# Performance work log

Hardware: AMD Instinct MI355X
Metric: run time of the kernel (lower is better)

Reference implementation:

```python
import jax, jax.numpy as jnp
import numpy as np

# Production-scale perfect decision-tree ensemble (Hummingbird perf_tree_trav layout)
B, F, T, D, C = 16384, 256, 512, 7, 4  # batch, features, trees, internal levels below root, classes


def setup_inputs() -> dict:
    key = jax.random.key(0)
    k = jax.random.split(key, 6)
    total = T * (2 ** (D + 1) - 2)  # concatenated per-level node/bias tables, level l has T*2^l entries
    return {
        "x": jax.random.normal(k[0], (B, F), dtype=jnp.float32),
        "root_nodes": jax.random.randint(k[1], (T,), 0, F, dtype=jnp.int32),
        "root_biases": jax.random.normal(k[2], (T,), dtype=jnp.float32),
        "tree_indices": jnp.arange(T, dtype=jnp.int32) * 2,
        "nodes_flat": jax.random.randint(k[3], (total,), 0, F, dtype=jnp.int32),
        "biases_flat": jax.random.normal(k[4], (total,), dtype=jnp.float32),
        "leaf_nodes": jax.random.normal(k[5], (T * 2 ** (D + 1), C), dtype=jnp.float32),
    }


def reference(x, root_nodes, root_biases, tree_indices, nodes_flat, biases_flat, leaf_nodes):
    # Root level: compare each tree's root feature against its bias. decision_cond = less (lt).
    # tree_indices = t*2 offsets indices into the flat level-1 table of size 2T;
    # the offset doubles along with the level size via `2*idx + cond`.
    idx = (x[:, root_nodes] < root_biases).astype(jnp.int32) + tree_indices  # [B, T]
    off = 0
    for l in range(1, D + 1):  # static loop over tree depth
        size = T << l
        lvl_nodes = nodes_flat[off:off + size]
        lvl_biases = biases_flat[off:off + size]
        feat_idx = lvl_nodes[idx]                          # [B, T] feature ids for current nodes
        feats = jnp.take_along_axis(x, feat_idx, axis=1)   # [B, T] per-sample feature gather
        idx = 2 * idx + (feats < lvl_biases[idx]).astype(jnp.int32)
        off += size
    leaves = leaf_nodes[idx]                               # [B, T, C]
    return leaves.sum(axis=1)                              # [B, C]
```

## Files before the change

### kernel.cpp

```cpp
#include <hip/hip_runtime.h>
#include <hip/hip_fp16.h>

#define BB 16384
#define FF 256
#define TT 512
#define DD 7

constexpr int NR1 = TT * 2;
constexpr int NR3 = TT * 8;
constexpr int NR5 = TT * 32;
constexpr int NN7 = TT * 128;
constexpr int NTOT = NR1 + NR3 + NR5 + NN7 + NN7;

constexpr size_t OFF_R3   = (size_t)NR1 * 16;
constexpr size_t OFF_R5   = OFF_R3 + (size_t)NR3 * 16;
constexpr size_t OFF_N7   = OFF_R5 + (size_t)NR5 * 16;
constexpr size_t OFF_LP   = OFF_N7 + (size_t)NN7 * 8;
constexpr size_t OFF_PART = OFF_LP + (size_t)NN7 * 16;
constexpr size_t WS_NEED  = OFF_PART + (size_t)2 * BB * 4 * sizeof(float);

__global__ void pack_kernel(const int* __restrict__ nf, const float* __restrict__ bf,
                            const float4* __restrict__ leaf4,
                            int4* __restrict__ R1, int4* __restrict__ R3,
                            int4* __restrict__ R5, int2* __restrict__ N7,
                            uint4* __restrict__ LP) {
    const int i = blockIdx.x * 256 + threadIdx.x;
    if (i < NR1) {
        const int e0 = i, eC = 2 * TT + 2 * i;
        const int fp = (nf[e0] & 255) | ((nf[eC] & 255) << 8) | ((nf[eC + 1] & 255) << 16);
        R1[i] = make_int4(fp, __float_as_int(bf[e0]),
                          __float_as_int(bf[eC]), __float_as_int(bf[eC + 1]));
    } else if (i < NR1 + NR3) {
        const int r = i - NR1;
        const int e0 = 6 * TT + r, eC = 14 * TT + 2 * r;
        const int fp = (nf[e0] & 255) | ((nf[eC] & 255) << 8) | ((nf[eC + 1] & 255) << 16);
        R3[r] = make_int4(fp, __float_as_int(bf[e0]),
                          __float_as_int(bf[eC]), __float_as_int(bf[eC + 1]));
    } else if (i < NR1 + NR3 + NR5) {
        const int r = i - NR1 - NR3;
        const int e0 = 30 * TT + r, eC = 62 * TT + 2 * r;
        const int fp = (nf[e0] & 255) | ((nf[eC] & 255) << 8) | ((nf[eC + 1] & 255) << 16);
        R5[r] = make_int4(fp, __float_as_int(bf[e0]),
                          __float_as_int(bf[eC]), __float_as_int(bf[eC + 1]));
    } else if (i < NR1 + NR3 + NR5 + NN7) {
        const int r = i - NR1 - NR3 - NR5;
        const int e = 126 * TT + r;
        N7[r] = make_int2(nf[e] & 255, __float_as_int(bf[e]));
    } else if (i < NTOT) {
        const int j = i - NR1 - NR3 - NR5 - NN7;
        const float4 l0 = leaf4[2 * j], l1 = leaf4[2 * j + 1];
        const __half2 a = __floats2half2_rn(l0.x, l0.y), b = __floats2half2_rn(l0.z, l0.w);
        const __half2 c = __floats2half2_rn(l1.x, l1.y), d = __floats2half2_rn(l1.z, l1.w);
        uint4 w;
        w.x = *reinterpret_cast<const unsigned int*>(&a);
        w.y = *reinterpret_cast<const unsigned int*>(&b);
        w.z = *reinterpret_cast<const unsigned int*>(&c);
        w.w = *reinterpret_cast<const unsigned int*>(&d);
        LP[j] = w;
    }
}

__device__ __forceinline__ int step2(const int4 w, const int i,
                                     const float* __restrict__ x_s,
                                     const int xb, const int sz) {
    const float v0 = x_s[xb | ((w.x & 255) ^ sz)];
    const int   c0 = (v0 < __int_as_float(w.y)) ? 1 : 0;
    const int   fc = c0 ? ((w.x >> 16) & 255) : ((w.x >> 8) & 255);
    const float bc = c0 ? __int_as_float(w.w) : __int_as_float(w.z);
    const float vc = x_s[xb | (fc ^ sz)];
    const int   c1 = (vc < bc) ? 1 : 0;
    return 4 * i + 2 * c0 + c1;
}

__global__ __launch_bounds__(1024, 4)
void tree_traverse_big(const float* __restrict__ x,
                       const int*   __restrict__ root_nodes,
                       const float* __restrict__ root_biases,
                       const int4*  __restrict__ R1, const int4* __restrict__ R3g,
                       const int4*  __restrict__ R5, const int2* __restrict__ N7,
                       const uint4* __restrict__ LP,
                       float*       __restrict__ out)
{
    extern __shared__ float smem[];
    float* x_s = smem;
    int4*  r3s = (int4*)(smem + 16384);

    const int tid = threadIdx.x;
    const int s   = tid & 63;
    const int tg  = tid >> 6;
    const int s0  = blockIdx.x * 64;

    {
        const float4* xg = (const float4*)(x + (size_t)s0 * FF);
        const int r  = tid >> 4;
        const int v  = tid & 15;
        const int rz = r & 31;
        float* row = x_s + (r << 8);
        #pragma unroll
        for (int c = 0; c < 4; ++c) {
            const float4 q = xg[r * (FF / 4) + v + 16 * c];
            const int f0 = (v + 16 * c) * 4;
            row[(f0 + 0) ^ rz] = q.x;
            row[(f0 + 1) ^ rz] = q.y;
            row[(f0 + 2) ^ rz] = q.z;
            row[(f0 + 3) ^ rz] = q.w;
        }
        #pragma unroll
        for (int i = 0; i < NR3 / 1024; ++i)
            r3s[tid + i * 1024] = R3g[tid + i * 1024];
    }
    __syncthreads();

    const int xb = s << 8;
    const int sz = s & 31;
    float a0 = 0.f, a1 = 0.f, a2 = 0.f, a3 = 0.f;

    constexpr int TPT = TT / 16;
    constexpr int NP  = 8;
    constexpr int NJ  = TPT / NP;

    #pragma unroll 1
    for (int j = 0; j < NJ; ++j) {
        const int tbase = tg * TPT + j * NP;
        int p[NP];

        #pragma unroll
        for (int k = 0; k < NP; ++k) {
            const int tu = __builtin_amdgcn_readfirstlane(tbase + k);
            const int   rn  = root_nodes[tu];
            const float rbv = root_biases[tu];
            const int4  rA  = R1[2 * tu];
            const int4  rB  = R1[2 * tu + 1];
            const int c0 = (x_s[xb | (rn ^ sz)] < rbv) ? 1 : 0;
            int4 r;
            r.x = c0 ? rB.x : rA.x;  r.y = c0 ? rB.y : rA.y;
            r.z = c0 ? rB.z : rA.z;  r.w = c0 ? rB.w : rA.w;
            p[k] = step2(r, c0, x_s, xb, sz);
        }
        #pragma unroll
        for (int k = 0; k < NP; ++k)
            p[k] = step2(r3s[((tbase + k) << 3) + p[k]], p[k], x_s, xb, sz);
        #pragma unroll
        for (int k = 0; k < NP; ++k)
            p[k] = step2(R5[((tbase + k) << 5) + p[k]], p[k], x_s, xb, sz);
        #pragma unroll
        for (int k = 0; k < NP; ++k) {
            const int idx7 = ((tbase + k) << 7) + p[k];
            const int2  n  = N7[idx7];
            const uint4 lp = LP[idx7];
            const int c7 = (x_s[xb | (n.x ^ sz)] < __int_as_float(n.y)) ? 1 : 0;
            const unsigned int w01 = c7 ? lp.z : lp.x;
            const unsigned int w23 = c7 ? lp.w : lp.y;
            const float2 f01 = __half22float2(*reinterpret_cast<const __half2*>(&w01));
            const float2 f23 = __half22float2(*reinterpret_cast<const __half2*>(&w23));
            a0 += f01.x; a1 += f01.y; a2 += f23.x; a3 += f23.y;
        }
    }

    __syncthreads();
    ((float4*)x_s)[tid] = make_float4(a0, a1, a2, a3);
    __syncthreads();
    if (tid < 256) {
        float o = 0.f;
        #pragma unroll
        for (int g = 0; g < 16; ++g)
            o += x_s[(g << 8) + tid];
        out[(size_t)s0 * 4 + tid] = o;
    }
}

__global__ __launch_bounds__(1024, 8)
void tree_traverse_kernel(const float* __restrict__ x,
                          const int*   __restrict__ root_nodes,
                          const float* __restrict__ root_biases,
                          const int4*  __restrict__ R1, const int4* __restrict__ R3,
                          const int4*  __restrict__ R5, const int2* __restrict__ N7,
                          const uint4* __restrict__ LP,
                          float*       __restrict__ part)
{
    extern __shared__ float x_s[];
    const int tid = threadIdx.x;
    const int s   = tid & 63;
    const int tg  = tid >> 6;
    const int s0  = blockIdx.x * 64;
    const int h0  = blockIdx.y * (TT / 2);
    {
        const float4* xg = (const float4*)(x + (size_t)s0 * FF);
        const int r = tid >> 4, v = tid & 15, rz = r & 31;
        float* row = x_s + (r << 8);
        #pragma unroll
        for (int c = 0; c < 4; ++c) {
            const float4 q = xg[r * (FF / 4) + v + 16 * c];
            const int f0 = (v + 16 * c) * 4;
            row[(f0 + 0) ^ rz] = q.x; row[(f0 + 1) ^ rz] = q.y;
            row[(f0 + 2) ^ rz] = q.z; row[(f0 + 3) ^ rz] = q.w;
        }
    }
    __syncthreads();
    const int xb = s << 8, sz = s & 31;
    float a0 = 0.f, a1 = 0.f, a2 = 0.f, a3 = 0.f;
    constexpr int TPT = (TT / 2) / 16, NP = 8, NJ = TPT / NP;
    #pragma unroll 1
    for (int j = 0; j < NJ; ++j) {
        const int tbase = h0 + tg * TPT + j * NP;
        int p[NP];
        #pragma unroll
        for (int k = 0; k < NP; ++k) {
            const int tu = __builtin_amdgcn_readfirstlane(tbase + k);
            const int   rn  = root_nodes[tu];
            const float rbv = root_biases[tu];
            const int4  rA  = R1[2 * tu];
            const int4  rB  = R1[2 * tu + 1];
            const int c0 = (x_s[xb | (rn ^ sz)] < rbv) ? 1 : 0;
            int4 r;
            r.x = c0 ? rB.x : rA.x;  r.y = c0 ? rB.y : rA.y;
            r.z = c0 ? rB.z : rA.z;  r.w = c0 ? rB.w : rA.w;
            p[k] = step2(r, c0, x_s, xb, sz);
        }
        #pragma unroll
        for (int k = 0; k < NP; ++k)
            p[k] = step2(R3[((tbase + k) << 3) + p[k]], p[k], x_s, xb, sz);
        #pragma unroll
        for (int k = 0; k < NP; ++k)
            p[k] = step2(R5[((tbase + k) << 5) + p[k]], p[k], x_s, xb, sz);
        #pragma unroll
        for (int k = 0; k < NP; ++k) {
            const int idx7 = ((tbase + k) << 7) + p[k];
            const int2  n  = N7[idx7];
            const uint4 lp = LP[idx7];
            const int c7 = (x_s[xb | (n.x ^ sz)] < __int_as_float(n.y)) ? 1 : 0;
            const unsigned int w01 = c7 ? lp.z : lp.x;
            const unsigned int w23 = c7 ? lp.w : lp.y;
            const float2 f01 = __half22float2(*reinterpret_cast<const __half2*>(&w01));
            const float2 f23 = __half22float2(*reinterpret_cast<const __half2*>(&w23));
            a0 += f01.x; a1 += f01.y; a2 += f23.x; a3 += f23.y;
        }
    }
    __syncthreads();
    ((float4*)x_s)[tid] = make_float4(a0, a1, a2, a3);
    __syncthreads();
    if (tid < 256) {
        float o = 0.f;
        #pragma unroll
        for (int g = 0; g < 16; ++g)
            o += x_s[(g << 8) + tid];
        part[((size_t)blockIdx.y * BB + s0) * 4 + tid] = o;
    }
}

__global__ void sum_kernel(const float4* __restrict__ part, float4* __restrict__ out) {
    const int i = blockIdx.x * 256 + threadIdx.x;
    if (i < BB) {
        const float4 a = part[i], b = part[BB + i];
        out[i] = make_float4(a.x + b.x, a.y + b.y, a.z + b.z, a.w + b.w);
    }
}

__global__ __launch_bounds__(1024, 4)
void tree_traverse_fallback(const float* __restrict__ x,
                            const int* __restrict__ root_nodes,
                            const float* __restrict__ root_biases,
                            const int* __restrict__ nodes_flat,
                            const float* __restrict__ biases_flat,
                            const float* __restrict__ leaf_nodes,
                            float* __restrict__ out)
{
    extern __shared__ float x_s[];
    const int tid = threadIdx.x;
    const int s = tid & 63, tg = tid >> 6;
    const int s0 = blockIdx.x * 64;
    {
        const float4* xg = (const float4*)(x + (size_t)s0 * FF);
        const int r = tid >> 4, v = tid & 15, rz = r & 31;
        float* row = x_s + (r << 8);
        #pragma unroll
        for (int c = 0; c < 4; ++c) {
            const float4 q = xg[r * (FF / 4) + v + 16 * c];
            const int f0 = (v + 16 * c) * 4;
            row[(f0 + 0) ^ rz] = q.x; row[(f0 + 1) ^ rz] = q.y;
            row[(f0 + 2) ^ rz] = q.z; row[(f0 + 3) ^ rz] = q.w;
        }
    }
    __syncthreads();
    const int xb = s << 8, sz = s & 31;
    const float4* leaf4 = (const float4*)leaf_nodes;
    float a0 = 0.f, a1 = 0.f, a2 = 0.f, a3 = 0.f;
    #pragma unroll 1
    for (int j = 0; j < 4; ++j) {
        const int tbase = tg * 32 + j * 8;
        int p[8];
        #pragma unroll
        for (int k = 0; k < 8; ++k) {
            const int t = tbase + k;
            p[k] = 2 * t + ((x_s[xb | (root_nodes[t] ^ sz)] < root_biases[t]) ? 1 : 0);
        }
        #pragma unroll
        for (int l = 1; l <= DD; ++l) {
            #pragma unroll
            for (int k = 0; k < 8; ++k) {
                const int fi = nodes_flat[p[k]];
                const float bi = biases_flat[p[k]];
                const int c = (x_s[xb | (fi ^ sz)] < bi) ? 1 : 0;
                p[k] = 2 * p[k] + 2 * TT + c;
            }
        }
        #pragma unroll
        for (int k = 0; k < 8; ++k) {
            const float4 lf = leaf4[p[k] - 254 * TT];
            a0 += lf.x; a1 += lf.y; a2 += lf.z; a3 += lf.w;
        }
    }
    __syncthreads();
    ((float4*)x_s)[tid] = make_float4(a0, a1, a2, a3);
    __syncthreads();
    if (tid < 256) {
        float o = 0.f;
        #pragma unroll
        for (int g = 0; g < 16; ++g) o += x_s[(g << 8) + tid];
        out[(size_t)s0 * 4 + tid] = o;
    }
}

extern "C" void kernel_launch(void* const* d_in, const int* in_sizes, int n_in,
                              void* d_out, int out_size, void* d_ws, size_t ws_size,
                              hipStream_t stream) {
    const float* x           = (const float*)d_in[0];
    const int*   root_nodes  = (const int*)  d_in[1];
    const float* root_biases = (const float*)d_in[2];
    const int*   nodes_flat  = (const int*)  d_in[4];
    const float* biases_flat = (const float*)d_in[5];
    const float* leaf_nodes  = (const float*)d_in[6];
    float*       out         = (float*)d_out;

    constexpr size_t LDS_SMALL = 65536;
    constexpr size_t LDS_BIG   = 131072;

    if (ws_size >= WS_NEED) {
        char* ws = (char*)d_ws;
        int4*  R1 = (int4*)ws;
        int4*  R3 = (int4*)(ws + OFF_R3);
        int4*  R5 = (int4*)(ws + OFF_R5);
        int2*  N7 = (int2*)(ws + OFF_N7);
        uint4* LP = (uint4*)(ws + OFF_LP);
        float* part = (float*)(ws + OFF_PART);

        pack_kernel<<<(NTOT + 255) / 256, 256, 0, stream>>>(
            nodes_flat, biases_flat, (const float4*)leaf_nodes, R1, R3, R5, N7, LP);

        int dev = 0;
        (void)hipGetDevice(&dev);
        int smCU = 0;
        (void)hipDeviceGetAttribute(&smCU,
                hipDeviceAttributeMaxSharedMemoryPerMultiprocessor, dev);
        bool big = false;
        if (smCU >= (int)LDS_BIG) {
            big = (hipFuncSetAttribute(
                       reinterpret_cast<const void*>(&tree_traverse_big),
                       hipFuncAttributeMaxDynamicSharedMemorySize,
                       (int)LDS_BIG) == hipSuccess);
        }

        if (big) {
            tree_traverse_big<<<BB / 64, 1024, LDS_BIG, stream>>>(
                x, root_nodes, root_biases, R1, R3, R5, N7, LP, out);
        } else {
            dim3 grid(BB / 64, 2);
            tree_traverse_kernel<<<grid, 1024, LDS_SMALL, stream>>>(
                x, root_nodes, root_biases, R1, R3, R5, N7, LP, part);
            sum_kernel<<<BB / 256, 256, 0, stream>>>((const float4*)part, (float4*)out);
        }
    } else {
        tree_traverse_fallback<<<BB / 64, 1024, LDS_SMALL, stream>>>(
            x, root_nodes, root_biases, nodes_flat, biases_flat, leaf_nodes, out);
    }
}
```

Measured before the change: 103.5 us.

## Split trees into four quarters per block with partial sums and reduction

Replaces the single big-LDS kernel, which processed all 512 trees per 64-sample block, with a 2D grid where each block handles a quarter of the trees. Each block now uses 80KB of LDS and holds only its quarter of the level-3 table, so two blocks can share a CU and there are four times as many blocks. Per-quarter partial sums go to the workspace and a generalized sum kernel adds them. The cost is reloading the x tile four times, an extra launch, and more workspace traffic.

```diff
diff --git a/kernel.cpp b/kernel.cpp
--- a/kernel.cpp
+++ b/kernel.cpp
@@ -17,7 +17,7 @@
 constexpr size_t OFF_N7   = OFF_R5 + (size_t)NR5 * 16;
 constexpr size_t OFF_LP   = OFF_N7 + (size_t)NN7 * 8;
 constexpr size_t OFF_PART = OFF_LP + (size_t)NN7 * 16;
-constexpr size_t WS_NEED  = OFF_PART + (size_t)2 * BB * 4 * sizeof(float);
+constexpr size_t WS_NEED  = OFF_PART + (size_t)4 * BB * 4 * sizeof(float);
 
 __global__ void pack_kernel(const int* __restrict__ nf, const float* __restrict__ bf,
                             const float4* __restrict__ leaf4,
@@ -72,14 +72,14 @@
     return 4 * i + 2 * c0 + c1;
 }
 
-__global__ __launch_bounds__(1024, 4)
-void tree_traverse_big(const float* __restrict__ x,
-                       const int*   __restrict__ root_nodes,
-                       const float* __restrict__ root_biases,
-                       const int4*  __restrict__ R1, const int4* __restrict__ R3g,
-                       const int4*  __restrict__ R5, const int2* __restrict__ N7,
-                       const uint4* __restrict__ LP,
-                       float*       __restrict__ out)
+__global__ __launch_bounds__(1024, 8)
+void tree_traverse_q(const float* __restrict__ x,
+                     const int*   __restrict__ root_nodes,
+                     const float* __restrict__ root_biases,
+                     const int4*  __restrict__ R1, const int4* __restrict__ R3g,
+                     const int4*  __restrict__ R5, const int2* __restrict__ N7,
+                     const uint4* __restrict__ LP,
+                     float*       __restrict__ part)
 {
     extern __shared__ float smem[];
     float* x_s = smem;
@@ -89,6 +89,8 @@
     const int s   = tid & 63;
     const int tg  = tid >> 6;
     const int s0  = blockIdx.x * 64;
+    const int q   = blockIdx.y;
+    const int h0  = q * (TT / 4);
 
     {
         const float4* xg = (const float4*)(x + (size_t)s0 * FF);
@@ -98,16 +100,14 @@
         float* row = x_s + (r << 8);
         #pragma unroll
         for (int c = 0; c < 4; ++c) {
-            const float4 q = xg[r * (FF / 4) + v + 16 * c];
+            const float4 qv = xg[r * (FF / 4) + v + 16 * c];
             const int f0 = (v + 16 * c) * 4;
-            row[(f0 + 0) ^ rz] = q.x;
-            row[(f0 + 1) ^ rz] = q.y;
-            row[(f0 + 2) ^ rz] = q.z;
-            row[(f0 + 3) ^ rz] = q.w;
-        }
-        #pragma unroll
-        for (int i = 0; i < NR3 / 1024; ++i)
-            r3s[tid + i * 1024] = R3g[tid + i * 1024];
+            row[(f0 + 0) ^ rz] = qv.x;
+            row[(f0 + 1) ^ rz] = qv.y;
+            row[(f0 + 2) ^ rz] = qv.z;
+            row[(f0 + 3) ^ rz] = qv.w;
+        }
+        r3s[tid] = R3g[(q << 10) + tid];
     }
     __syncthreads();
 
@@ -115,46 +115,40 @@
     const int sz = s & 31;
     float a0 = 0.f, a1 = 0.f, a2 = 0.f, a3 = 0.f;
 
-    constexpr int TPT = TT / 16;
-    constexpr int NP  = 8;
-    constexpr int NJ  = TPT / NP;
-
-    #pragma unroll 1
-    for (int j = 0; j < NJ; ++j) {
-        const int tbase = tg * TPT + j * NP;
-        int p[NP];
-
-        #pragma unroll
-        for (int k = 0; k < NP; ++k) {
-            const int tu = __builtin_amdgcn_readfirstlane(tbase + k);
-            const int   rn  = root_nodes[tu];
-            const float rbv = root_biases[tu];
-            const int4  rA  = R1[2 * tu];
-            const int4  rB  = R1[2 * tu + 1];
-            const int c0 = (x_s[xb | (rn ^ sz)] < rbv) ? 1 : 0;
-            int4 r;
-            r.x = c0 ? rB.x : rA.x;  r.y = c0 ? rB.y : rA.y;
-            r.z = c0 ? rB.z : rA.z;  r.w = c0 ? rB.w : rA.w;
-            p[k] = step2(r, c0, x_s, xb, sz);
-        }
-        #pragma unroll
-        for (int k = 0; k < NP; ++k)
-            p[k] = step2(r3s[((tbase + k) << 3) + p[k]], p[k], x_s, xb, sz);
-        #pragma unroll
-        for (int k = 0; k < NP; ++k)
-            p[k] = step2(R5[((tbase + k) << 5) + p[k]], p[k], x_s, xb, sz);
-        #pragma unroll
-        for (int k = 0; k < NP; ++k) {
-            const int idx7 = ((tbase + k) << 7) + p[k];
-            const int2  n  = N7[idx7];
-            const uint4 lp = LP[idx7];
-            const int c7 = (x_s[xb | (n.x ^ sz)] < __int_as_float(n.y)) ? 1 : 0;
-            const unsigned int w01 = c7 ? lp.z : lp.x;
-            const unsigned int w23 = c7 ? lp.w : lp.y;
-            const float2 f01 = __half22float2(*reinterpret_cast<const __half2*>(&w01));
-            const float2 f23 = __half22float2(*reinterpret_cast<const __half2*>(&w23));
-            a0 += f01.x; a1 += f01.y; a2 += f23.x; a3 += f23.y;
-        }
+    constexpr int NP = 8;
+    const int lt0 = tg * NP;
+    int p[NP];
+
+    #pragma unroll
+    for (int k = 0; k < NP; ++k) {
+        const int tu = __builtin_amdgcn_readfirstlane(h0 + lt0 + k);
+        const int   rn  = root_nodes[tu];
+        const float rbv = root_biases[tu];
+        const int4  rA  = R1[2 * tu];
+        const int4  rB  = R1[2 * tu + 1];
+        const int c0 = (x_s[xb | (rn ^ sz)] < rbv) ? 1 : 0;
+        int4 r;
+        r.x = c0 ? rB.x : rA.x;  r.y = c0 ? rB.y : rA.y;
+        r.z = c0 ? rB.z : rA.z;  r.w = c0 ? rB.w : rA.w;
+        p[k] = step2(r, c0, x_s, xb, sz);
+    }
+    #pragma unroll
+    for (int k = 0; k < NP; ++k)
+        p[k] = step2(r3s[((lt0 + k) << 3) + p[k]], p[k], x_s, xb, sz);
+    #pragma unroll
+    for (int k = 0; k < NP; ++k)
+        p[k] = step2(R5[((h0 + lt0 + k) << 5) + p[k]], p[k], x_s, xb, sz);
+    #pragma unroll
+    for (int k = 0; k < NP; ++k) {
+        const int idx7 = ((h0 + lt0 + k) << 7) + p[k];
+        const int2  n  = N7[idx7];
+        const uint4 lp = LP[idx7];
+        const int c7 = (x_s[xb | (n.x ^ sz)] < __int_as_float(n.y)) ? 1 : 0;
+        const unsigned int w01 = c7 ? lp.z : lp.x;
+        const unsigned int w23 = c7 ? lp.w : lp.y;
+        const float2 f01 = __half22float2(*reinterpret_cast<const __half2*>(&w01));
+        const float2 f23 = __half22float2(*reinterpret_cast<const __half2*>(&w23));
+        a0 += f01.x; a1 += f01.y; a2 += f23.x; a3 += f23.y;
     }
 
     __syncthreads();
@@ -165,7 +159,20 @@
         #pragma unroll
         for (int g = 0; g < 16; ++g)
             o += x_s[(g << 8) + tid];
-        out[(size_t)s0 * 4 + tid] = o;
+        part[((size_t)q * BB + s0) * 4 + tid] = o;
+    }
+}
+
+__global__ void sum_kernel(const float4* __restrict__ part, float4* __restrict__ out,
+                           int nparts) {
+    const int i = blockIdx.x * 256 + threadIdx.x;
+    if (i < BB) {
+        float4 o = part[i];
+        for (int q = 1; q < nparts; ++q) {
+            const float4 a = part[(size_t)q * BB + i];
+            o.x += a.x; o.y += a.y; o.z += a.z; o.w += a.w;
+        }
+        out[i] = o;
     }
 }
 
@@ -248,14 +255,6 @@
     }
 }
 
-__global__ void sum_kernel(const float4* __restrict__ part, float4* __restrict__ out) {
-    const int i = blockIdx.x * 256 + threadIdx.x;
-    if (i < BB) {
-        const float4 a = part[i], b = part[BB + i];
-        out[i] = make_float4(a.x + b.x, a.y + b.y, a.z + b.z, a.w + b.w);
-    }
-}
-
 __global__ __launch_bounds__(1024, 4)
 void tree_traverse_fallback(const float* __restrict__ x,
                             const int* __restrict__ root_nodes,
@@ -333,7 +332,7 @@
     float*       out         = (float*)d_out;
 
     constexpr size_t LDS_SMALL = 65536;
-    constexpr size_t LDS_BIG   = 131072;
+    constexpr size_t LDS_Q     = 65536 + 16384;
 
     if (ws_size >= WS_NEED) {
         char* ws = (char*)d_ws;
@@ -352,22 +351,24 @@
         int smCU = 0;
         (void)hipDeviceGetAttribute(&smCU,
                 hipDeviceAttributeMaxSharedMemoryPerMultiprocessor, dev);
-        bool big = false;
-        if (smCU >= (int)LDS_BIG) {
-            big = (hipFuncSetAttribute(
-                       reinterpret_cast<const void*>(&tree_traverse_big),
+        bool qok = false;
+        if (smCU >= (int)(2 * LDS_Q)) {
+            qok = (hipFuncSetAttribute(
+                       reinterpret_cast<const void*>(&tree_traverse_q),
                        hipFuncAttributeMaxDynamicSharedMemorySize,
-                       (int)LDS_BIG) == hipSuccess);
-        }
-
-        if (big) {
-            tree_traverse_big<<<BB / 64, 1024, LDS_BIG, stream>>>(
-                x, root_nodes, root_biases, R1, R3, R5, N7, LP, out);
+                       (int)LDS_Q) == hipSuccess);
+        }
+
+        if (qok) {
+            dim3 grid(BB / 64, 4);
+            tree_traverse_q<<<grid, 1024, LDS_Q, stream>>>(
+                x, root_nodes, root_biases, R1, R3, R5, N7, LP, part);
+            sum_kernel<<<BB / 256, 256, 0, stream>>>((const float4*)part, (float4*)out, 4);
         } else {
             dim3 grid(BB / 64, 2);
             tree_traverse_kernel<<<grid, 1024, LDS_SMALL, stream>>>(
                 x, root_nodes, root_biases, R1, R3, R5, N7, LP, part);
-            sum_kernel<<<BB / 256, 256, 0, stream>>>((const float4*)part, (float4*)out);
+            sum_kernel<<<BB / 256, 256, 0, stream>>>((const float4*)part, (float4*)out, 2);
         }
     } else {
         tree_traverse_fallback<<<BB / 64, 1024, LDS_SMALL, stream>>>(
```

Result: faster. 99.08 us (-4.3%).
